# Kernel tuning notes

Hardware: AMD Instinct MI355X
Metric: run time of the kernel (lower is better)

## Reference

```python
import jax, jax.numpy as jnp
import numpy as np

# sym2 (== db2) decomposition filters from pywt
_DEC_LO = np.array([-0.12940952255126037, 0.22414386804185735,
                    0.8365163037378079, 0.48296291314453416], dtype=np.float32)
_DEC_HI = np.array([-0.48296291314453416, 0.8365163037378079,
                    -0.22414386804185735, -0.12940952255126037], dtype=np.float32)
# pytorch_wavelets flips the filters before torch's cross-correlation conv
H0R = jnp.asarray(_DEC_LO[::-1].copy())
H1R = jnp.asarray(_DEC_HI[::-1].copy())
L = 4  # filter length
LEVEL = 3


def afb1d(x):
    """One level of DWT (mode='zero'), x: (B, C, N) -> (lo, hi) each (B, C, (N+L-1)//2)."""
    N = x.shape[-1]
    out = (N + L - 1) // 2              # pywt dwt_coeff_len for mode='zero'
    p = 2 * (out - 1) - N + L           # total pad
    if p % 2 == 1:                      # odd-length signals get one extra zero at the end
        x = jnp.pad(x, ((0, 0), (0, 0), (0, 1)))
    ph = p // 2
    x = jnp.pad(x, ((0, 0), (0, 0), (ph, ph)))
    # strided windows: y[n] = sum_k h[k] * x_pad[2n + k]
    wins = [x[..., k:k + 2 * out:2][..., :out] for k in range(L)]
    lo = sum(H0R[k] * wins[k] for k in range(L))
    hi = sum(H1R[k] * wins[k] for k in range(L))
    return lo, hi


def wavelet_packet(x, level=LEVEL):
    # breadth-first, lo-first ordering == lexicographic sort of 'a'/'d' paths
    bands = [x]
    for _ in range(level):
        nxt = []
        for b in bands:
            lo, hi = afb1d(b)
            nxt.append(lo)
            nxt.append(hi)
        bands = nxt
    return bands


def setup_inputs() -> dict:
    key = jax.random.key(0)
    k1, k2, k3 = jax.random.split(key, 3)
    B, C, N, num_classes = 131072, 3, 50, 5
    total_features = 192  # 8 leaves * 3 channels * 8 samples
    x = jax.random.normal(k1, (B, C, N), dtype=jnp.float32)
    W = jax.random.normal(k2, (num_classes, total_features), dtype=jnp.float32) * 0.05
    b = jax.random.normal(k3, (num_classes,), dtype=jnp.float32) * 0.05
    return {"x": x, "W": W, "b": b}


def reference(x, W, b):
    bands = wavelet_packet(x)
    B = x.shape[0]
    feats = jnp.concatenate([band.reshape(B, -1) for band in bands], axis=1)  # (B, 192)
    return feats @ W.T + b                          # (B, 5)
```

## Files before the change

kernel.cpp:

```cpp
#include <hip/hip_runtime.h>

struct Amat { float a[64][50]; };

constexpr Amat makeA() {
    constexpr float h0[4] = { 0.48296291314453416f,  0.8365163037378079f,
                              0.22414386804185735f, -0.12940952255126037f};
    constexpr float h1[4] = {-0.12940952255126037f, -0.22414386804185735f,
                              0.8365163037378079f,  -0.48296291314453416f};
    float L1[2][26][50] = {};
    for (int band = 0; band < 2; ++band)
        for (int m = 0; m < 26; ++m)
            for (int n = 0; n < 50; ++n) {
                int k = n - 2 * m + 2;
                L1[band][m][n] = (k >= 0 && k < 4) ? (band ? h1[k] : h0[k]) : 0.0f;
            }
    float L2[4][14][50] = {};
    for (int j = 0; j < 4; ++j)
        for (int m = 0; m < 14; ++m)
            for (int n = 0; n < 50; ++n) {
                float acc = 0.0f;
                for (int k = 0; k < 4; ++k) {
                    int p = 2 * m + k - 2;
                    if (p >= 0 && p < 26)
                        acc += (j & 1 ? h1[k] : h0[k]) * L1[j >> 1][p][n];
                }
                L2[j][m][n] = acc;
            }
    Amat A = {};
    for (int j = 0; j < 8; ++j)
        for (int m = 0; m < 8; ++m)
            for (int n = 0; n < 50; ++n) {
                float acc = 0.0f;
                for (int k = 0; k < 4; ++k) {
                    int p = 2 * m + k - 2;
                    if (p >= 0 && p < 14)
                        acc += (j & 1 ? h1[k] : h0[k]) * L2[j >> 1][p][n];
                }
                A.a[j * 8 + m][n] = acc;
            }
    return A;
}

__device__ __constant__ Amat cA = makeA();

__global__ __launch_bounds__(256) void build_M(const float* __restrict__ W,
                                               float* __restrict__ Mg) {
    __shared__ float sW[960];
    const int tid = threadIdx.x;
    #pragma unroll
    for (int t = 0; t < 4; ++t) {
        const int idx = tid + t * 256;
        if (idx < 960) sW[idx] = W[idx];
    }
    __syncthreads();

    const int i = tid;
    if (i >= 150) return;
    const int c = i / 50, n = i - c * 50;
    float acc0 = 0.f, acc1 = 0.f, acc2 = 0.f, acc3 = 0.f, acc4 = 0.f;
    #pragma unroll 16
    for (int f = 0; f < 64; ++f) {
        const float av = cA.a[f][n];
        const int wj = (f >> 3) * 24 + c * 8 + (f & 7);
        acc0 = fmaf(sW[0 * 192 + wj], av, acc0);
        acc1 = fmaf(sW[1 * 192 + wj], av, acc1);
        acc2 = fmaf(sW[2 * 192 + wj], av, acc2);
        acc3 = fmaf(sW[3 * 192 + wj], av, acc3);
        acc4 = fmaf(sW[4 * 192 + wj], av, acc4);
    }
    const int g = i >> 1, p = i & 1;
    float* dst = &Mg[g * 12 + p * 5];
    dst[0] = acc0; dst[1] = acc1; dst[2] = acc2; dst[3] = acc3; dst[4] = acc4;
}

__global__ __launch_bounds__(256) void dwt_gemv(const float* __restrict__ x,
                                                const float* __restrict__ Mg,
                                                const float* __restrict__ bias,
                                                float* __restrict__ out) {
    __shared__ float sM[75 * 12];
    const int tid = threadIdx.x;
    for (int idx = tid; idx < 900; idx += 256) sM[idx] = Mg[idx];
    __syncthreads();

    const size_t r = (size_t)blockIdx.x * 256 + tid;
    const float2* __restrict__ xr = (const float2*)(x + r * 150);

    float a0 = 0.f, a1 = 0.f, a2 = 0.f, a3 = 0.f, a4 = 0.f;
    #pragma unroll 25
    for (int g = 0; g < 75; ++g) {
        const float2 xv = xr[g];
        const float4 m0 = *(const float4*)&sM[g * 12 + 0];
        const float4 m1 = *(const float4*)&sM[g * 12 + 4];
        const float2 m2 = *(const float2*)&sM[g * 12 + 8];
        a0 = fmaf(m0.x, xv.x, a0);
        a1 = fmaf(m0.y, xv.x, a1);
        a2 = fmaf(m0.z, xv.x, a2);
        a3 = fmaf(m0.w, xv.x, a3);
        a4 = fmaf(m1.x, xv.x, a4);
        a0 = fmaf(m1.y, xv.y, a0);
        a1 = fmaf(m1.z, xv.y, a1);
        a2 = fmaf(m1.w, xv.y, a2);
        a3 = fmaf(m2.x, xv.y, a3);
        a4 = fmaf(m2.y, xv.y, a4);
    }

    float* o = &out[r * 5];
    o[0] = a0 + bias[0];
    o[1] = a1 + bias[1];
    o[2] = a2 + bias[2];
    o[3] = a3 + bias[3];
    o[4] = a4 + bias[4];
}

extern "C" void kernel_launch(void* const* d_in, const int* in_sizes, int n_in,
                              void* d_out, int out_size, void* d_ws, size_t ws_size,
                              hipStream_t stream) {
    const float* x    = (const float*)d_in[0];
    const float* W    = (const float*)d_in[1];
    const float* bias = (const float*)d_in[2];
    float*       out  = (float*)d_out;
    float*       Mg   = (float*)d_ws;

    build_M<<<1, 256, 0, stream>>>(W, Mg);

    const int B = in_sizes[0] / 150;
    dwt_gemv<<<B / 256, 256, 0, stream>>>(x, Mg, bias, out);
}
```

Baseline: 28.98 us.

## Fuse filter-matrix build into GEMV kernel, two rows per thread with float4 loads

Removes the separate single-block build_M launch: every block now recomputes the 150x5 folded wavelet-times-W matrix into shared memory, so there is no inter-kernel dependency or workspace round trip. Each thread handles two consecutive rows (300 floats) with 16-byte float4 loads, and prefetches the first 8 vectors before the matrix build so the global loads overlap that setup. This adds redundant per-block compute of the matrix (150 threads x 64 iterations) and doubles per-thread register and work load, which halves the number of threads in flight.

```diff
diff --git a/kernel.cpp b/kernel.cpp
--- a/kernel.cpp
+++ b/kernel.cpp
@@ -43,10 +43,26 @@
 
 __device__ __constant__ Amat cA = makeA();
 
-__global__ __launch_bounds__(256) void build_M(const float* __restrict__ W,
-                                               float* __restrict__ Mg) {
+#define FMA_EL(A0,A1,A2,A3,A4, xv, ib)            \
+    A0 = fmaf(sM[(ib) * 5 + 0], (xv), A0);        \
+    A1 = fmaf(sM[(ib) * 5 + 1], (xv), A1);        \
+    A2 = fmaf(sM[(ib) * 5 + 2], (xv), A2);        \
+    A3 = fmaf(sM[(ib) * 5 + 3], (xv), A3);        \
+    A4 = fmaf(sM[(ib) * 5 + 4], (xv), A4);
+
+__global__ __launch_bounds__(256) void dwt_fused(const float* __restrict__ x,
+                                                 const float* __restrict__ W,
+                                                 const float* __restrict__ bias,
+                                                 float* __restrict__ out) {
     __shared__ float sW[960];
+    __shared__ float sM[752];
     const int tid = threadIdx.x;
+    const size_t r0 = (size_t)blockIdx.x * 512 + 2 * (size_t)tid;
+    const float4* __restrict__ xr = (const float4*)(x + r0 * 150);
+
+    float4 q0 = xr[0], q1 = xr[1], q2 = xr[2], q3 = xr[3];
+    float4 q4 = xr[4], q5 = xr[5], q6 = xr[6], q7 = xr[7];
+
     #pragma unroll
     for (int t = 0; t < 4; ++t) {
         const int idx = tid + t * 256;
@@ -54,62 +70,67 @@
     }
     __syncthreads();
 
-    const int i = tid;
-    if (i >= 150) return;
-    const int c = i / 50, n = i - c * 50;
-    float acc0 = 0.f, acc1 = 0.f, acc2 = 0.f, acc3 = 0.f, acc4 = 0.f;
-    #pragma unroll 16
-    for (int f = 0; f < 64; ++f) {
-        const float av = cA.a[f][n];
-        const int wj = (f >> 3) * 24 + c * 8 + (f & 7);
-        acc0 = fmaf(sW[0 * 192 + wj], av, acc0);
-        acc1 = fmaf(sW[1 * 192 + wj], av, acc1);
-        acc2 = fmaf(sW[2 * 192 + wj], av, acc2);
-        acc3 = fmaf(sW[3 * 192 + wj], av, acc3);
-        acc4 = fmaf(sW[4 * 192 + wj], av, acc4);
+    if (tid < 150) {
+        const int c = tid / 50, n = tid - c * 50;
+        float m0 = 0.f, m1 = 0.f, m2 = 0.f, m3 = 0.f, m4 = 0.f;
+        #pragma unroll 16
+        for (int f = 0; f < 64; ++f) {
+            const float av = cA.a[f][n];
+            const int wj = (f >> 3) * 24 + c * 8 + (f & 7);
+            m0 = fmaf(sW[0 * 192 + wj], av, m0);
+            m1 = fmaf(sW[1 * 192 + wj], av, m1);
+            m2 = fmaf(sW[2 * 192 + wj], av, m2);
+            m3 = fmaf(sW[3 * 192 + wj], av, m3);
+            m4 = fmaf(sW[4 * 192 + wj], av, m4);
+        }
+        float* dst = &sM[tid * 5];
+        dst[0] = m0; dst[1] = m1; dst[2] = m2; dst[3] = m3; dst[4] = m4;
     }
-    const int g = i >> 1, p = i & 1;
-    float* dst = &Mg[g * 12 + p * 5];
-    dst[0] = acc0; dst[1] = acc1; dst[2] = acc2; dst[3] = acc3; dst[4] = acc4;
-}
-
-__global__ __launch_bounds__(256) void dwt_gemv(const float* __restrict__ x,
-                                                const float* __restrict__ Mg,
-                                                const float* __restrict__ bias,
-                                                float* __restrict__ out) {
-    __shared__ float sM[75 * 12];
-    const int tid = threadIdx.x;
-    for (int idx = tid; idx < 900; idx += 256) sM[idx] = Mg[idx];
     __syncthreads();
 
-    const size_t r = (size_t)blockIdx.x * 256 + tid;
-    const float2* __restrict__ xr = (const float2*)(x + r * 150);
+    float a0 = 0.f, a1 = 0.f, a2 = 0.f, a3 = 0.f, a4 = 0.f;
+    float b0 = 0.f, b1 = 0.f, b2 = 0.f, b3 = 0.f, b4 = 0.f;
 
-    float a0 = 0.f, a1 = 0.f, a2 = 0.f, a3 = 0.f, a4 = 0.f;
-    #pragma unroll 25
-    for (int g = 0; g < 75; ++g) {
-        const float2 xv = xr[g];
-        const float4 m0 = *(const float4*)&sM[g * 12 + 0];
-        const float4 m1 = *(const float4*)&sM[g * 12 + 4];
-        const float2 m2 = *(const float2*)&sM[g * 12 + 8];
-        a0 = fmaf(m0.x, xv.x, a0);
-        a1 = fmaf(m0.y, xv.x, a1);
-        a2 = fmaf(m0.z, xv.x, a2);
-        a3 = fmaf(m0.w, xv.x, a3);
-        a4 = fmaf(m1.x, xv.x, a4);
-        a0 = fmaf(m1.y, xv.y, a0);
-        a1 = fmaf(m1.z, xv.y, a1);
-        a2 = fmaf(m1.w, xv.y, a2);
-        a3 = fmaf(m2.x, xv.y, a3);
-        a4 = fmaf(m2.y, xv.y, a4);
+    {
+        const float4 qs[8] = {q0, q1, q2, q3, q4, q5, q6, q7};
+        #pragma unroll
+        for (int j = 0; j < 8; ++j) {
+            const float4 q = qs[j];
+            FMA_EL(a0,a1,a2,a3,a4, q.x, 4*j + 0)
+            FMA_EL(a0,a1,a2,a3,a4, q.y, 4*j + 1)
+            FMA_EL(a0,a1,a2,a3,a4, q.z, 4*j + 2)
+            FMA_EL(a0,a1,a2,a3,a4, q.w, 4*j + 3)
+        }
+    }
+    #pragma unroll 8
+    for (int j = 8; j < 37; ++j) {
+        const float4 q = xr[j];
+        FMA_EL(a0,a1,a2,a3,a4, q.x, 4*j + 0)
+        FMA_EL(a0,a1,a2,a3,a4, q.y, 4*j + 1)
+        FMA_EL(a0,a1,a2,a3,a4, q.z, 4*j + 2)
+        FMA_EL(a0,a1,a2,a3,a4, q.w, 4*j + 3)
+    }
+    {
+        const float4 q = xr[37];
+        FMA_EL(a0,a1,a2,a3,a4, q.x, 148)
+        FMA_EL(a0,a1,a2,a3,a4, q.y, 149)
+        FMA_EL(b0,b1,b2,b3,b4, q.z, 0)
+        FMA_EL(b0,b1,b2,b3,b4, q.w, 1)
+    }
+    #pragma unroll 8
+    for (int j = 38; j < 75; ++j) {
+        const float4 q = xr[j];
+        const int ib = 4*j - 150;
+        FMA_EL(b0,b1,b2,b3,b4, q.x, ib + 0)
+        FMA_EL(b0,b1,b2,b3,b4, q.y, ib + 1)
+        FMA_EL(b0,b1,b2,b3,b4, q.z, ib + 2)
+        FMA_EL(b0,b1,b2,b3,b4, q.w, ib + 3)
     }
 
-    float* o = &out[r * 5];
-    o[0] = a0 + bias[0];
-    o[1] = a1 + bias[1];
-    o[2] = a2 + bias[2];
-    o[3] = a3 + bias[3];
-    o[4] = a4 + bias[4];
+    const float c0 = bias[0], c1 = bias[1], c2 = bias[2], c3 = bias[3], c4 = bias[4];
+    float* o = out + r0 * 5;
+    o[0] = a0 + c0;  o[1] = a1 + c1;  o[2] = a2 + c2;  o[3] = a3 + c3;  o[4] = a4 + c4;
+    o[5] = b0 + c0;  o[6] = b1 + c1;  o[7] = b2 + c2;  o[8] = b3 + c3;  o[9] = b4 + c4;
 }
 
 extern "C" void kernel_launch(void* const* d_in, const int* in_sizes, int n_in,
@@ -119,10 +140,7 @@
     const float* W    = (const float*)d_in[1];
     const float* bias = (const float*)d_in[2];
     float*       out  = (float*)d_out;
-    float*       Mg   = (float*)d_ws;
-
-    build_M<<<1, 256, 0, stream>>>(W, Mg);
 
     const int B = in_sizes[0] / 150;
-    dwt_gemv<<<B / 256, 256, 0, stream>>>(x, Mg, bias, out);
+    dwt_fused<<<B / 512, 256, 0, stream>>>(x, W, bias, out);
 }
```

Result: faster. 27.60 us (-4.7%).

## Fuse M-matrix build into GEMV kernel and split each row across four lanes

Applied to the files above, without the earlier changes.

Drops the separate build_M launch. Every block now recomputes the 150x5 folded wavelet+linear matrix into shared memory, then runs the GEMV. Each row is handled by four lanes, which read interleaved float2 chunks for coalesced loads, and the partial sums are combined with xor shuffles. This removes a kernel launch and the strided per-thread row access. The cost is redundant M computation in every block (64 FMAs per element, 750 elements, 2048 blocks) and four times as many threads.

```diff
diff --git a/kernel.cpp b/kernel.cpp
--- a/kernel.cpp
+++ b/kernel.cpp
@@ -43,73 +43,83 @@
 
 __device__ __constant__ Amat cA = makeA();
 
-__global__ __launch_bounds__(256) void build_M(const float* __restrict__ W,
-                                               float* __restrict__ Mg) {
-    __shared__ float sW[960];
+#define SWP 193
+
+#define FMA_EL(xv, ib)                          \
+    a0 = fmaf(sM[(ib) * 5 + 0], (xv), a0);      \
+    a1 = fmaf(sM[(ib) * 5 + 1], (xv), a1);      \
+    a2 = fmaf(sM[(ib) * 5 + 2], (xv), a2);      \
+    a3 = fmaf(sM[(ib) * 5 + 3], (xv), a3);      \
+    a4 = fmaf(sM[(ib) * 5 + 4], (xv), a4);
+
+__global__ __launch_bounds__(256) void dwt_fused(const float* __restrict__ x,
+                                                 const float* __restrict__ W,
+                                                 const float* __restrict__ bias,
+                                                 float* __restrict__ out) {
+    __shared__ float sW[5 * SWP];
+    __shared__ float sM[752];
     const int tid = threadIdx.x;
+    const size_t g   = (size_t)blockIdx.x * 256 + tid;
+    const size_t row = g >> 2;
+    const int    q   = (int)(g & 3);
+
+    const float2* __restrict__ xr = (const float2*)(x + row * 150);
+
+    float2 v[19];
+    #pragma unroll
+    for (int j = 0; j < 18; ++j) v[j] = xr[4 * j + q];
+    v[18] = xr[(q < 3) ? (72 + q) : 74];
+
     #pragma unroll
     for (int t = 0; t < 4; ++t) {
         const int idx = tid + t * 256;
-        if (idx < 960) sW[idx] = W[idx];
+        if (idx < 960) sW[(idx / 192) * SWP + (idx % 192)] = W[idx];
     }
     __syncthreads();
 
-    const int i = tid;
-    if (i >= 150) return;
-    const int c = i / 50, n = i - c * 50;
-    float acc0 = 0.f, acc1 = 0.f, acc2 = 0.f, acc3 = 0.f, acc4 = 0.f;
-    #pragma unroll 16
-    for (int f = 0; f < 64; ++f) {
-        const float av = cA.a[f][n];
-        const int wj = (f >> 3) * 24 + c * 8 + (f & 7);
-        acc0 = fmaf(sW[0 * 192 + wj], av, acc0);
-        acc1 = fmaf(sW[1 * 192 + wj], av, acc1);
-        acc2 = fmaf(sW[2 * 192 + wj], av, acc2);
-        acc3 = fmaf(sW[3 * 192 + wj], av, acc3);
-        acc4 = fmaf(sW[4 * 192 + wj], av, acc4);
+    #pragma unroll
+    for (int t = 0; t < 3; ++t) {
+        const int p = tid + t * 256;
+        if (p < 750) {
+            const int i = p / 5, k = p - 5 * i;
+            const int c = i / 50, n = i - 50 * c;
+            float acc = 0.f;
+            #pragma unroll 16
+            for (int f = 0; f < 64; ++f)
+                acc = fmaf(sW[k * SWP + (f >> 3) * 24 + c * 8 + (f & 7)],
+                           cA.a[f][n], acc);
+            sM[p] = acc;
+        }
     }
-    const int g = i >> 1, p = i & 1;
-    float* dst = &Mg[g * 12 + p * 5];
-    dst[0] = acc0; dst[1] = acc1; dst[2] = acc2; dst[3] = acc3; dst[4] = acc4;
-}
-
-__global__ __launch_bounds__(256) void dwt_gemv(const float* __restrict__ x,
-                                                const float* __restrict__ Mg,
-                                                const float* __restrict__ bias,
-                                                float* __restrict__ out) {
-    __shared__ float sM[75 * 12];
-    const int tid = threadIdx.x;
-    for (int idx = tid; idx < 900; idx += 256) sM[idx] = Mg[idx];
     __syncthreads();
 
-    const size_t r = (size_t)blockIdx.x * 256 + tid;
-    const float2* __restrict__ xr = (const float2*)(x + r * 150);
-
     float a0 = 0.f, a1 = 0.f, a2 = 0.f, a3 = 0.f, a4 = 0.f;
-    #pragma unroll 25
-    for (int g = 0; g < 75; ++g) {
-        const float2 xv = xr[g];
-        const float4 m0 = *(const float4*)&sM[g * 12 + 0];
-        const float4 m1 = *(const float4*)&sM[g * 12 + 4];
-        const float2 m2 = *(const float2*)&sM[g * 12 + 8];
-        a0 = fmaf(m0.x, xv.x, a0);
-        a1 = fmaf(m0.y, xv.x, a1);
-        a2 = fmaf(m0.z, xv.x, a2);
-        a3 = fmaf(m0.w, xv.x, a3);
-        a4 = fmaf(m1.x, xv.x, a4);
-        a0 = fmaf(m1.y, xv.y, a0);
-        a1 = fmaf(m1.z, xv.y, a1);
-        a2 = fmaf(m1.w, xv.y, a2);
-        a3 = fmaf(m2.x, xv.y, a3);
-        a4 = fmaf(m2.y, xv.y, a4);
+    #pragma unroll
+    for (int j = 0; j < 18; ++j) {
+        const int ib = 2 * (4 * j + q);
+        FMA_EL(v[j].x, ib)
+        FMA_EL(v[j].y, ib + 1)
+    }
+    if (q < 3) {
+        const int ib = 2 * (72 + q);
+        FMA_EL(v[18].x, ib)
+        FMA_EL(v[18].y, ib + 1)
     }
 
-    float* o = &out[r * 5];
-    o[0] = a0 + bias[0];
-    o[1] = a1 + bias[1];
-    o[2] = a2 + bias[2];
-    o[3] = a3 + bias[3];
-    o[4] = a4 + bias[4];
+    a0 += __shfl_xor(a0, 1); a0 += __shfl_xor(a0, 2);
+    a1 += __shfl_xor(a1, 1); a1 += __shfl_xor(a1, 2);
+    a2 += __shfl_xor(a2, 1); a2 += __shfl_xor(a2, 2);
+    a3 += __shfl_xor(a3, 1); a3 += __shfl_xor(a3, 2);
+    a4 += __shfl_xor(a4, 1); a4 += __shfl_xor(a4, 2);
+
+    if (q == 0) {
+        float* o = out + row * 5;
+        o[0] = a0 + bias[0];
+        o[1] = a1 + bias[1];
+        o[2] = a2 + bias[2];
+        o[3] = a3 + bias[3];
+        o[4] = a4 + bias[4];
+    }
 }
 
 extern "C" void kernel_launch(void* const* d_in, const int* in_sizes, int n_in,
@@ -119,10 +129,8 @@
     const float* W    = (const float*)d_in[1];
     const float* bias = (const float*)d_in[2];
     float*       out  = (float*)d_out;
-    float*       Mg   = (float*)d_ws;
-
-    build_M<<<1, 256, 0, stream>>>(W, Mg);
 
     const int B = in_sizes[0] / 150;
-    dwt_gemv<<<B / 256, 256, 0, stream>>>(x, Mg, bias, out);
+    const int grid = (B * 4) / 256;
+    dwt_fused<<<grid, 256, 0, stream>>>(x, W, bias, out);
 }
```

Measured after the change: 30.55 us. 1.05x slower.

## Coalesce row loads with 16-lane cooperative dot products and shuffle reduction

Applied to the files above, without the earlier changes.

Replaces the one-thread-per-row GEMV with 16-lane groups that each process two rows. Lanes read consecutive float2 elements so global loads are coalesced, then combine partial sums with xor shuffles. M is re-laid out class-major with bias folded into the workspace, and outputs are staged in shared memory for a coalesced store. The cost is more blocks, each repeating the shared-memory load of M, plus extra shuffle and sync overhead.

```diff
diff --git a/kernel.cpp b/kernel.cpp
--- a/kernel.cpp
+++ b/kernel.cpp
@@ -44,6 +44,7 @@
 __device__ __constant__ Amat cA = makeA();
 
 __global__ __launch_bounds__(256) void build_M(const float* __restrict__ W,
+                                               const float* __restrict__ bias,
                                                float* __restrict__ Mg) {
     __shared__ float sW[960];
     const int tid = threadIdx.x;
@@ -54,62 +55,104 @@
     }
     __syncthreads();
 
-    const int i = tid;
-    if (i >= 150) return;
-    const int c = i / 50, n = i - c * 50;
-    float acc0 = 0.f, acc1 = 0.f, acc2 = 0.f, acc3 = 0.f, acc4 = 0.f;
-    #pragma unroll 16
-    for (int f = 0; f < 64; ++f) {
-        const float av = cA.a[f][n];
-        const int wj = (f >> 3) * 24 + c * 8 + (f & 7);
-        acc0 = fmaf(sW[0 * 192 + wj], av, acc0);
-        acc1 = fmaf(sW[1 * 192 + wj], av, acc1);
-        acc2 = fmaf(sW[2 * 192 + wj], av, acc2);
-        acc3 = fmaf(sW[3 * 192 + wj], av, acc3);
-        acc4 = fmaf(sW[4 * 192 + wj], av, acc4);
+    if (tid < 150) {
+        const int c = tid / 50, n = tid - c * 50;
+        float m0 = 0.f, m1 = 0.f, m2 = 0.f, m3 = 0.f, m4 = 0.f;
+        #pragma unroll 16
+        for (int f = 0; f < 64; ++f) {
+            const float av = cA.a[f][n];
+            const int wj = (f >> 3) * 24 + c * 8 + (f & 7);
+            m0 = fmaf(sW[0 * 192 + wj], av, m0);
+            m1 = fmaf(sW[1 * 192 + wj], av, m1);
+            m2 = fmaf(sW[2 * 192 + wj], av, m2);
+            m3 = fmaf(sW[3 * 192 + wj], av, m3);
+            m4 = fmaf(sW[4 * 192 + wj], av, m4);
+        }
+        Mg[0 * 160 + tid] = m0;
+        Mg[1 * 160 + tid] = m1;
+        Mg[2 * 160 + tid] = m2;
+        Mg[3 * 160 + tid] = m3;
+        Mg[4 * 160 + tid] = m4;
+    } else if (tid < 160) {
+        #pragma unroll
+        for (int k = 0; k < 5; ++k) Mg[k * 160 + tid] = 0.f;
+    } else if (tid < 165) {
+        Mg[800 + (tid - 160)] = bias[tid - 160];
     }
-    const int g = i >> 1, p = i & 1;
-    float* dst = &Mg[g * 12 + p * 5];
-    dst[0] = acc0; dst[1] = acc1; dst[2] = acc2; dst[3] = acc3; dst[4] = acc4;
 }
+
+#define RPB2 32
 
 __global__ __launch_bounds__(256) void dwt_gemv(const float* __restrict__ x,
                                                 const float* __restrict__ Mg,
-                                                const float* __restrict__ bias,
                                                 float* __restrict__ out) {
-    __shared__ float sM[75 * 12];
+    __shared__ float sM[805];
+    __shared__ float sO[RPB2 * 5];
     const int tid = threadIdx.x;
-    for (int idx = tid; idx < 900; idx += 256) sM[idx] = Mg[idx];
+    #pragma unroll
+    for (int t = 0; t < 4; ++t) {
+        const int idx = tid + t * 256;
+        if (idx < 805) sM[idx] = Mg[idx];
+    }
     __syncthreads();
 
-    const size_t r = (size_t)blockIdx.x * 256 + tid;
-    const float2* __restrict__ xr = (const float2*)(x + r * 150);
+    const int g  = tid >> 4;
+    const int lg = tid & 15;
+    const size_t rA = (size_t)blockIdx.x * RPB2 + g;
+    const size_t rB = rA + 16;
+    const float2* __restrict__ xa = (const float2*)(x + rA * 150);
+    const float2* __restrict__ xb = (const float2*)(x + rB * 150);
 
     float a0 = 0.f, a1 = 0.f, a2 = 0.f, a3 = 0.f, a4 = 0.f;
-    #pragma unroll 25
-    for (int g = 0; g < 75; ++g) {
-        const float2 xv = xr[g];
-        const float4 m0 = *(const float4*)&sM[g * 12 + 0];
-        const float4 m1 = *(const float4*)&sM[g * 12 + 4];
-        const float2 m2 = *(const float2*)&sM[g * 12 + 8];
-        a0 = fmaf(m0.x, xv.x, a0);
-        a1 = fmaf(m0.y, xv.x, a1);
-        a2 = fmaf(m0.z, xv.x, a2);
-        a3 = fmaf(m0.w, xv.x, a3);
-        a4 = fmaf(m1.x, xv.x, a4);
-        a0 = fmaf(m1.y, xv.y, a0);
-        a1 = fmaf(m1.z, xv.y, a1);
-        a2 = fmaf(m1.w, xv.y, a2);
-        a3 = fmaf(m2.x, xv.y, a3);
-        a4 = fmaf(m2.y, xv.y, a4);
+    float b0 = 0.f, b1 = 0.f, b2 = 0.f, b3 = 0.f, b4 = 0.f;
+
+    #pragma unroll
+    for (int j = 0; j < 5; ++j) {
+        const int fi = j * 16 + lg;
+        if (fi < 75) {
+            const float2 xva = xa[fi];
+            const float2 xvb = xb[fi];
+            const int d = 2 * fi;
+            { const float2 m = *(const float2*)&sM[0 * 160 + d];
+              a0 = fmaf(m.x, xva.x, a0); a0 = fmaf(m.y, xva.y, a0);
+              b0 = fmaf(m.x, xvb.x, b0); b0 = fmaf(m.y, xvb.y, b0); }
+            { const float2 m = *(const float2*)&sM[1 * 160 + d];
+              a1 = fmaf(m.x, xva.x, a1); a1 = fmaf(m.y, xva.y, a1);
+              b1 = fmaf(m.x, xvb.x, b1); b1 = fmaf(m.y, xvb.y, b1); }
+            { const float2 m = *(const float2*)&sM[2 * 160 + d];
+              a2 = fmaf(m.x, xva.x, a2); a2 = fmaf(m.y, xva.y, a2);
+              b2 = fmaf(m.x, xvb.x, b2); b2 = fmaf(m.y, xvb.y, b2); }
+            { const float2 m = *(const float2*)&sM[3 * 160 + d];
+              a3 = fmaf(m.x, xva.x, a3); a3 = fmaf(m.y, xva.y, a3);
+              b3 = fmaf(m.x, xvb.x, b3); b3 = fmaf(m.y, xvb.y, b3); }
+            { const float2 m = *(const float2*)&sM[4 * 160 + d];
+              a4 = fmaf(m.x, xva.x, a4); a4 = fmaf(m.y, xva.y, a4);
+              b4 = fmaf(m.x, xvb.x, b4); b4 = fmaf(m.y, xvb.y, b4); }
+        }
     }
 
-    float* o = &out[r * 5];
-    o[0] = a0 + bias[0];
-    o[1] = a1 + bias[1];
-    o[2] = a2 + bias[2];
-    o[3] = a3 + bias[3];
-    o[4] = a4 + bias[4];
+    #pragma unroll
+    for (int o = 1; o < 16; o <<= 1) {
+        a0 += __shfl_xor(a0, o); a1 += __shfl_xor(a1, o);
+        a2 += __shfl_xor(a2, o); a3 += __shfl_xor(a3, o);
+        a4 += __shfl_xor(a4, o);
+        b0 += __shfl_xor(b0, o); b1 += __shfl_xor(b1, o);
+        b2 += __shfl_xor(b2, o); b3 += __shfl_xor(b3, o);
+        b4 += __shfl_xor(b4, o);
+    }
+
+    if (lg == 0) {
+        float* oa = &sO[g * 5];
+        oa[0] = a0 + sM[800]; oa[1] = a1 + sM[801]; oa[2] = a2 + sM[802];
+        oa[3] = a3 + sM[803]; oa[4] = a4 + sM[804];
+        float* ob = &sO[(g + 16) * 5];
+        ob[0] = b0 + sM[800]; ob[1] = b1 + sM[801]; ob[2] = b2 + sM[802];
+        ob[3] = b3 + sM[803]; ob[4] = b4 + sM[804];
+    }
+    __syncthreads();
+
+    if (tid < RPB2 * 5)
+        out[(size_t)blockIdx.x * (RPB2 * 5) + tid] = sO[tid];
 }
 
 extern "C" void kernel_launch(void* const* d_in, const int* in_sizes, int n_in,
@@ -121,8 +164,9 @@
     float*       out  = (float*)d_out;
     float*       Mg   = (float*)d_ws;
 
-    build_M<<<1, 256, 0, stream>>>(W, Mg);
+    build_M<<<1, 256, 0, stream>>>(W, bias, Mg);
 
-    const int B = in_sizes[0] / 150;
-    dwt_gemv<<<B / 256, 256, 0, stream>>>(x, Mg, bias, out);
+    const int B    = in_sizes[0] / 150;
+    const int grid = B / RPB2;
+    dwt_gemv<<<grid, 256, 0, stream>>>(x, Mg, out);
 }
```

Result: no change. 28.83 us (-0.5%).
